# Performance work log

Measured on AMD Instinct MI355X. Metric: run time of the kernel, lower is better.

Reference implementation:

```python
import jax, jax.numpy as jnp
import numpy as np

N = 100_000          # nodes
E = 3_200_000        # edges (avg degree 32)
NEG_SLOPE = 0.2      # PyG GATConv default


def _gat_conv(x, src, dst, W, a_src, a_dst, b, n):
    """Single-head PyG-style GATConv. src/dst already include self-loops."""
    h = x @ W                                   # [N, F_out]
    logits = (h @ a_src)[src] + (h @ a_dst)[dst]  # [E']
    e = jax.nn.leaky_relu(logits, NEG_SLOPE)
    m = jax.ops.segment_max(e, dst, num_segments=n)
    ex = jnp.exp(e - m[dst])                    # stable ragged softmax over in-edges
    s = jax.ops.segment_sum(ex, dst, num_segments=n)
    alpha = ex / (s[dst] + 1e-16)
    out = jax.ops.segment_sum(h[src] * alpha[:, None], dst, num_segments=n)
    return out + b


def setup_inputs() -> dict:
    key = jax.random.key(0)
    ks = jax.random.split(key, 20)
    x = jax.random.normal(ks[0], (N, 3), dtype=jnp.float32)
    edge_index = jax.random.randint(ks[1], (2, E), 0, N, dtype=jnp.int64)

    def lin(k, fin, fout):
        return jax.random.normal(k, (fin, fout), dtype=jnp.float32) * (1.0 / np.sqrt(fin))

    def att(k, f):
        return jax.random.normal(k, (f,), dtype=jnp.float32) * (1.0 / np.sqrt(f))

    inp = {"x": x, "edge_index": edge_index}
    # forward-direction convs
    inp["W1"], inp["as1"], inp["ad1"], inp["b1"] = lin(ks[2], 3, 16), att(ks[3], 16), att(ks[4], 16), jnp.zeros((16,), jnp.float32)
    inp["W2"], inp["as2"], inp["ad2"], inp["b2"] = lin(ks[5], 16, 1), att(ks[6], 1), att(ks[7], 1), jnp.zeros((1,), jnp.float32)
    # reverse-direction convs
    inp["W1r"], inp["as1r"], inp["ad1r"], inp["b1r"] = lin(ks[8], 3, 16), att(ks[9], 16), att(ks[10], 16), jnp.zeros((16,), jnp.float32)
    inp["W2r"], inp["as2r"], inp["ad2r"], inp["b2r"] = lin(ks[11], 16, 1), att(ks[12], 1), att(ks[13], 1), jnp.zeros((1,), jnp.float32)
    return inp


def reference(x, edge_index, W1, as1, ad1, b1, W2, as2, ad2, b2,
              W1r, as1r, ad1r, b1r, W2r, as2r, ad2r, b2r):
    n = x.shape[0]
    loops = jnp.arange(n, dtype=edge_index.dtype)
    # forward direction (self-loops appended, as PyG add_self_loops=True)
    src = jnp.concatenate([edge_index[0], loops])
    dst = jnp.concatenate([edge_index[1], loops])
    # reverse direction: stack([ei[1], ei[0]]) then self-loops
    rsrc = jnp.concatenate([edge_index[1], loops])
    rdst = jnp.concatenate([edge_index[0], loops])

    xf = jax.nn.relu(_gat_conv(x, src, dst, W1, as1, ad1, b1, n))
    xf = _gat_conv(xf, src, dst, W2, as2, ad2, b2, n)

    xr = jax.nn.relu(_gat_conv(x, rsrc, rdst, W1r, as1r, ad1r, b1r, n))
    xr = _gat_conv(xr, rsrc, rdst, W2r, as2r, ad2r, b2r, n)

    return (xf + xr) * 0.5
```

## Files before the change

kernel.cpp:

```cpp
#include <hip/hip_runtime.h>
#include <math.h>

#define NSLOPE 0.2f
#define BSH 8
#define BNODES 256
#define NID_MASK 0x1FFFF
#define SENT 0xFFFFFFFFu
#define CAP 10240
#define GB 768
#define RE 2560
#define SLOT 12
#define SPILLCAP 256
#define BN9 512
#define LCAP 18432
#define BAGT 1024
#define CPP9 9

__device__ __forceinline__ float lrelu(float v) { return v > 0.f ? v : NSLOPE * v; }

__global__ void k_prep(const float* __restrict__ x,
                       const float* __restrict__ as1, const float* __restrict__ ad1,
                       const float* __restrict__ as1r, const float* __restrict__ ad1r,
                       const float* __restrict__ W1, const float* __restrict__ W1r,
                       float4* __restrict__ rec4f, float4* __restrict__ rec4r,
                       float* __restrict__ s1df, float* __restrict__ s1dr,
                       int* __restrict__ gcur, int NS, int N) {
    int i = blockIdx.x * blockDim.x + threadIdx.x;
    if (i < NS) gcur[i] = 0;
    if (i >= N) return;
    float x0 = x[3 * i], x1 = x[3 * i + 1], x2 = x[3 * i + 2];
    float ssf = 0.f, sdf = 0.f, ssr = 0.f, sdr = 0.f;
#pragma unroll
    for (int k = 0; k < 16; k++) {
        float hf = x0 * W1[k] + x1 * W1[16 + k] + x2 * W1[32 + k];
        ssf += hf * as1[k];
        sdf += hf * ad1[k];
        float hr = x0 * W1r[k] + x1 * W1r[16 + k] + x2 * W1r[32 + k];
        ssr += hr * as1r[k];
        sdr += hr * ad1r[k];
    }
    rec4f[i] = make_float4(x0, x1, x2, ssf);
    rec4r[i] = make_float4(x0, x1, x2, ssr);
    s1df[i] = sdf; s1dr[i] = sdr;
}

__global__ void __launch_bounds__(512) k_scatsort(
        const void* __restrict__ ei, long long E,
        int NB, int NS, int* __restrict__ gcur, unsigned* __restrict__ bin) {
    extern __shared__ unsigned smem[];
    unsigned* slots = smem;
    int* cnt  = (int*)(slots + (size_t)NS * SLOT);
    int* gpos = cnt + NS;
    int* spill_s = gpos + NS;
    int* spill_p = spill_s + SPILLCAP;
    unsigned* spill_r = (unsigned*)(spill_p + SPILLCAP);
    int* spn = (int*)(spill_r + SPILLCAP);
    __shared__ int flagsm;

    int t = threadIdx.x;
    if (t < 64) {
        const unsigned long long* p = (const unsigned long long*)ei;
        bool bad = false;
#pragma unroll
        for (int i = 0; i < 4; i++)
            if (p[t * 4 + i] >= (1ull << 32)) bad = true;
        unsigned long long mask = __ballot(bad);
        if (t == 0) flagsm = (mask == 0ull) ? 1 : 0;
    }
    __syncthreads();
    int fl = flagsm;
    long long chunk = (E + GB - 1) / GB;
    long long cstart = (long long)blockIdx.x * chunk;
    long long cend = cstart + chunk; if (cend > E) cend = E;

    for (long long rs = cstart; rs < cend; rs += RE) {
        int ne = (int)min((long long)RE, cend - rs);
        for (int c = t; c < NS; c += 512) cnt[c] = 0;
        if (t == 0) *spn = 0;
        __syncthreads();
#pragma unroll
        for (int k = 0; k < RE / 512; k++) {
            int idx = t + k * 512;
            if (idx < ne) {
                long long i = rs + idx;
                int u, v;
                if (fl) { const long long* p = (const long long*)ei; u = (int)p[i]; v = (int)p[E + i]; }
                else    { const int* p = (const int*)ei; u = p[i]; v = p[E + i]; }
                unsigned r0 = (unsigned)u | ((unsigned)(v & (BNODES - 1)) << 17);
                int s0 = v >> BSH;
                unsigned r1 = (unsigned)v | ((unsigned)(u & (BNODES - 1)) << 17);
                int s1 = NB + (u >> BSH);
                int p0 = atomicAdd(&cnt[s0], 1);
                if (p0 < SLOT) slots[s0 * SLOT + p0] = r0;
                else { int sp = atomicAdd(spn, 1); if (sp < SPILLCAP) { spill_s[sp] = s0; spill_p[sp] = p0; spill_r[sp] = r0; } }
                int p1 = atomicAdd(&cnt[s1], 1);
                if (p1 < SLOT) slots[s1 * SLOT + p1] = r1;
                else { int sp = atomicAdd(spn, 1); if (sp < SPILLCAP) { spill_s[sp] = s1; spill_p[sp] = p1; spill_r[sp] = r1; } }
            }
        }
        __syncthreads();
        for (int c = t; c < NS; c += 512) {
            int n = cnt[c];
            int rn = (n + 1) & ~1;
            gpos[c] = rn ? atomicAdd(&gcur[c], rn) : 0;
        }
        __syncthreads();
        for (int c = t; c < NS; c += 512) {
            int n = cnt[c];
            if (!n) continue;
            int rn = (n + 1) & ~1;
            int g = gpos[c];
            long long b = (long long)c * CAP;
            int m = n < SLOT ? n : SLOT;
            if (g + rn <= CAP) {
                uint2* bp = (uint2*)(bin + b + g);
                int np = (m + 1) >> 1;
                for (int j = 0; j < np; j++) {
                    unsigned v0 = slots[c * SLOT + 2 * j];
                    unsigned v1 = (2 * j + 1 < m) ? slots[c * SLOT + 2 * j + 1] : SENT;
                    bp[j] = make_uint2(v0, v1);
                }
                if (n > SLOT && rn > n)
                    bin[b + g + n] = SENT;
            }
        }
        int nsp = *spn; if (nsp > SPILLCAP) nsp = SPILLCAP;
        for (int i = t; i < nsp; i += 512) {
            int s = spill_s[i];
            int off = gpos[s] + spill_p[i];
            if (off < CAP) bin[(long long)s * CAP + off] = spill_r[i];
        }
        __syncthreads();
    }
}

__global__ void __launch_bounds__(BAGT, 8) k_bagg1(
        unsigned* __restrict__ bin, const int* __restrict__ gcur,
        const float4* __restrict__ rec4f, const float* __restrict__ s1df,
        const float4* __restrict__ rec4r, const float* __restrict__ s1dr,
        const float* __restrict__ b1, const float* __restrict__ W1,
        const float* __restrict__ W2,
        const float* __restrict__ as2, const float* __restrict__ ad2,
        const float* __restrict__ b1r, const float* __restrict__ W1r,
        const float* __restrict__ W2r,
        const float* __restrict__ as2r, const float* __restrict__ ad2r,
        float2* __restrict__ p2f, float* __restrict__ s2df,
        float2* __restrict__ p2r, float* __restrict__ s2dr,
        int* __restrict__ aoff, int* __restrict__ aend, int NB8, int N) {
    int bb = blockIdx.x, dir = blockIdx.y;
    const float4* rec4 = dir ? rec4r : rec4f;
    const float* s1d = dir ? s1dr : s1df;
    const float* b1_ = dir ? b1r : b1;
    const float* W1_ = dir ? W1r : W1;
    const float* W2_ = dir ? W2r : W2;
    float as2v = dir ? as2r[0] : as2[0];
    float ad2v = dir ? ad2r[0] : ad2[0];
    float2* p2 = dir ? p2r : p2f;
    float* s2d = dir ? s2dr : s2df;

    int c0 = dir * NB8 + 2 * bb;
    bool c1ok = (2 * bb + 1) < NB8;
    long long base = (long long)c0 * CAP;
    int n0 = gcur[c0]; if (n0 > CAP) n0 = CAP;
    int n1 = c1ok ? gcur[c0 + 1] : 0; if (n1 > CAP) n1 = CAP;
    int npair0 = n0 >> 1, npair1 = n1 >> 1;
    if (npair0 > LCAP / 2) npair0 = LCAP / 2;
    if (npair0 + npair1 > LCAP / 2) npair1 = LCAP / 2 - npair0;
    int nptot = npair0 + npair1;
    int v0 = bb << 9;
    int nv = N - v0; if (nv > BN9) nv = BN9;

    __shared__ int cnt[BN9];
    __shared__ int loff[BN9];
    __shared__ int segtot[8];
    __shared__ unsigned lds_u[LCAP];
    int t = threadIdx.x;

    const uint2* bp0 = (const uint2*)(bin + base);
    const uint2* bp1 = (const uint2*)(bin + base) + CAP / 2;
    uint2 recs[CPP9];
#pragma unroll
    for (int k = 0; k < CPP9; k++) {
        int i = t + k * BAGT;
        uint2 r = make_uint2(SENT, SENT);
        if (i < npair0) r = bp0[i];
        else if (i < nptot) {
            r = bp1[i - npair0];
            if (r.x != SENT) r.x += (256u << 17);
            if (r.y != SENT) r.y += (256u << 17);
        }
        recs[k] = r;
    }
    if (t < BN9) cnt[t] = 0;
    __syncthreads();
#pragma unroll
    for (int k = 0; k < CPP9; k++) {
        if (recs[k].x != SENT) atomicAdd(&cnt[recs[k].x >> 17], 1);
        if (recs[k].y != SENT) atomicAdd(&cnt[recs[k].y >> 17], 1);
    }
    __syncthreads();
    if (t < BN9) {
        int lane = t & 63, wv = t >> 6;
        int val = cnt[t];
        int incl = val;
#pragma unroll
        for (int od = 1; od < 64; od <<= 1) {
            int up = __shfl_up(incl, od);
            if (lane >= od) incl += up;
        }
        if (lane == 63) segtot[wv] = incl;
        loff[t] = incl - val;
    }
    __syncthreads();
    if (t < BN9) {
        int wv = t >> 6;
        int offs = 0;
#pragma unroll
        for (int j = 0; j < 8; j++) offs += (j < wv) ? segtot[j] : 0;
        int ex = loff[t] + offs;
        loff[t] = ex;
        cnt[t] = ex;
    }
    __syncthreads();
#pragma unroll
    for (int k = 0; k < CPP9; k++) {
        if (recs[k].x != SENT) {
            int p = atomicAdd(&cnt[recs[k].x >> 17], 1);
            lds_u[p] = recs[k].x & NID_MASK;
        }
        if (recs[k].y != SENT) {
            int p = atomicAdd(&cnt[recs[k].y >> 17], 1);
            lds_u[p] = recs[k].y & NID_MASK;
        }
    }
    __syncthreads();
    int node = t >> 1, lane = t & 1;
    float sdv = (node < nv) ? s1d[v0 + node] : 0.f;
    float d = 0.f, a0 = 0.f, a1 = 0.f, a2 = 0.f;
    if (node < nv) {
        int ls = loff[node], le = cnt[node];
        for (int pos = ls + lane; pos < le; pos += 2) {
            unsigned u = lds_u[pos];
            float4 r = rec4[u];
            float w = __expf(lrelu(r.w + sdv));
            d += w; a0 += w * r.x; a1 += w * r.y; a2 += w * r.z;
        }
    }
    d  += __shfl_xor(d, 1);
    a0 += __shfl_xor(a0, 1);
    a1 += __shfl_xor(a1, 1);
    a2 += __shfl_xor(a2, 1);
    if (lane == 0 && node < nv) {
        int v = v0 + node;
        float4 r = rec4[v];
        float w = __expf(lrelu(r.w + sdv));
        float dd = d + w;
        float inv = 1.f / (dd + 1e-16f);
        float m0 = (a0 + w * r.x) * inv;
        float m1 = (a1 + w * r.y) * inv;
        float m2 = (a2 + w * r.z) * inv;
        float h2v = 0.f;
#pragma unroll
        for (int k = 0; k < 16; k++) {
            float o = m0 * W1_[k] + m1 * W1_[16 + k] + m2 * W1_[32 + k] + b1_[k];
            o = fmaxf(o, 0.f);
            h2v += o * W2_[k];
        }
        p2[v] = make_float2(h2v, h2v * as2v);
        s2d[v] = h2v * ad2v;
    }
    int nreal = (nv > 0) ? cnt[nv - 1] : 0;
    if (t == 0 && (nreal & 1)) lds_u[nreal] = SENT;
    __syncthreads();
    int ndp = (nreal + 1) >> 1;
    uint2* bq = (uint2*)(bin + base);
    for (int i = t; i < ndp; i += BAGT)
        bq[i] = make_uint2(lds_u[2 * i], lds_u[2 * i + 1]);
    if (t < nv) {
        aoff[dir * N + v0 + t] = (int)(base + loff[t]);
        aend[dir * N + v0 + t] = (int)(base + cnt[t]);
    }
}

__global__ void k_agg2(const unsigned* __restrict__ bin,
                       const int* __restrict__ aoff, const int* __restrict__ aend,
                       const float2* __restrict__ p2f, const float* __restrict__ s2df,
                       const float2* __restrict__ p2r, const float* __restrict__ s2dr,
                       const float* __restrict__ b2, const float* __restrict__ b2r,
                       float* __restrict__ out, int N) {
    int tid = blockIdx.x * blockDim.x + threadIdx.x;
    int v = tid >> 3;
    int lane = tid & 7;
    if (v >= N) return;
    float res[2];
#pragma unroll
    for (int dir = 0; dir < 2; dir++) {
        const float2* p2 = dir ? p2r : p2f;
        const float* s2d = dir ? s2dr : s2df;
        float bias = dir ? b2r[0] : b2[0];
        float sd = s2d[v];
        int st = aoff[dir * N + v], en = aend[dir * N + v];
        float d = 0.f, a = 0.f;
        if (lane == 0) {
            float2 ts = p2[v];
            float w = __expf(lrelu(ts.y + sd));
            d = w; a = w * ts.x;
        }
        int j = st + lane;
        for (; j + 24 < en; j += 32) {
            unsigned u0 = __builtin_nontemporal_load(bin + j);
            unsigned u1 = __builtin_nontemporal_load(bin + j + 8);
            unsigned u2 = __builtin_nontemporal_load(bin + j + 16);
            unsigned u3 = __builtin_nontemporal_load(bin + j + 24);
            float2 t0 = p2[u0];
            float2 t1 = p2[u1];
            float2 t2 = p2[u2];
            float2 t3 = p2[u3];
            float w0 = __expf(lrelu(t0.y + sd));
            float w1 = __expf(lrelu(t1.y + sd));
            float w2 = __expf(lrelu(t2.y + sd));
            float w3 = __expf(lrelu(t3.y + sd));
            d += (w0 + w1) + (w2 + w3);
            a += w0 * t0.x + w1 * t1.x + w2 * t2.x + w3 * t3.x;
        }
        for (; j < en; j += 8) {
            unsigned u = __builtin_nontemporal_load(bin + j);
            float2 t = p2[u];
            float w = __expf(lrelu(t.y + sd));
            d += w;
            a += w * t.x;
        }
#pragma unroll
        for (int mask = 1; mask < 8; mask <<= 1) {
            d += __shfl_xor(d, mask);
            a += __shfl_xor(a, mask);
        }
        res[dir] = a / (d + 1e-16f) + bias;
    }
    if (lane == 0) out[v] = 0.5f * (res[0] + res[1]);
}

extern "C" void kernel_launch(void* const* d_in, const int* in_sizes, int n_in,
                              void* d_out, int out_size, void* d_ws, size_t ws_size,
                              hipStream_t stream) {
    const float* x   = (const float*)d_in[0];
    const void*  ei  = d_in[1];
    const float* W1  = (const float*)d_in[2];
    const float* as1 = (const float*)d_in[3];
    const float* ad1 = (const float*)d_in[4];
    const float* b1  = (const float*)d_in[5];
    const float* W2  = (const float*)d_in[6];
    const float* as2 = (const float*)d_in[7];
    const float* ad2 = (const float*)d_in[8];
    const float* b2  = (const float*)d_in[9];
    const float* W1r  = (const float*)d_in[10];
    const float* as1r = (const float*)d_in[11];
    const float* ad1r = (const float*)d_in[12];
    const float* b1r  = (const float*)d_in[13];
    const float* W2r  = (const float*)d_in[14];
    const float* as2r = (const float*)d_in[15];
    const float* ad2r = (const float*)d_in[16];
    const float* b2r  = (const float*)d_in[17];

    const int N = in_sizes[0] / 3;
    const long long E = in_sizes[1] / 2;
    const int NB8 = (N + BNODES - 1) >> BSH;
    const int NS = 2 * NB8;
    const int NB9 = (N + BN9 - 1) >> 9;

    char* w = (char*)d_ws;
    size_t o = 0;
    auto A = [&](size_t bytes) { o = (o + 255) & ~(size_t)255; size_t r = o; o += bytes; return r; };
    size_t oR4f  = A(sizeof(float4) * N);
    size_t oR4r  = A(sizeof(float4) * N);
    size_t oS1df = A(sizeof(float) * N);
    size_t oS1dr = A(sizeof(float) * N);
    size_t oP2f  = A(sizeof(float2) * N);
    size_t oS2df = A(sizeof(float) * N);
    size_t oP2r  = A(sizeof(float2) * N);
    size_t oS2dr = A(sizeof(float) * N);
    size_t oAoff = A(sizeof(int) * 2 * N);
    size_t oAend = A(sizeof(int) * 2 * N);
    size_t oGcur = A(sizeof(int) * NS);
    size_t oBin  = A(sizeof(unsigned) * (size_t)NS * CAP);
    (void)ws_size; (void)n_in; (void)out_size;

    float4* rec4f = (float4*)(w + oR4f);
    float4* rec4r = (float4*)(w + oR4r);
    float*  s1df = (float*)(w + oS1df);
    float*  s1dr = (float*)(w + oS1dr);
    float2* p2f  = (float2*)(w + oP2f);
    float*  s2df = (float*)(w + oS2df);
    float2* p2r  = (float2*)(w + oP2r);
    float*  s2dr = (float*)(w + oS2dr);
    int*    aoff = (int*)(w + oAoff);
    int*    aend = (int*)(w + oAend);
    int*    gcur = (int*)(w + oGcur);
    unsigned* bin = (unsigned*)(w + oBin);

    dim3 gN((N + 255) / 256);
    dim3 gAgg1(NB9, 2);
    dim3 gAgg2((N * 8 + 255) / 256);

    size_t smem = sizeof(unsigned) * (size_t)NS * SLOT
                + sizeof(int) * (size_t)NS * 2
                + sizeof(int) * SPILLCAP * 2
                + sizeof(unsigned) * SPILLCAP
                + 64;

    k_prep<<<gN, 256, 0, stream>>>(x, as1, ad1, as1r, ad1r, W1, W1r,
                                   rec4f, rec4r, s1df, s1dr, gcur, NS, N);
    k_scatsort<<<GB, 512, smem, stream>>>(ei, E, NB8, NS, gcur, bin);
    k_bagg1<<<gAgg1, BAGT, 0, stream>>>(bin, gcur, rec4f, s1df, rec4r, s1dr,
                                        b1, W1, W2, as2, ad2,
                                        b1r, W1r, W2r, as2r, ad2r,
                                        p2f, s2df, p2r, s2dr, aoff, aend, NB8, N);
    k_agg2<<<gAgg2, 256, 0, stream>>>(bin, aoff, aend, p2f, s2df, p2r, s2dr,
                                      b2, b2r, (float*)d_out, N);
}
```

Measured before the change: 234.9 us.

## Pack scatter bins densely and widen per-node aggregation to 16 lanes

The scatter-sort stops padding each block's per-bucket chunk to an even length, so no sentinel holes are written into the bins. Odd global offsets are handled with a scalar head and tail store. The segmented aggregator now masks the trailing odd element itself. Scatter grid, edges-per-block and slot sizes are retuned, and the final aggregation uses 16 lanes per node with 2-way unrolling instead of 8 lanes with 4-way. Denser bins mean fewer records to read and sort, at the cost of misaligned scalar stores and more lanes idle on low-degree nodes.

```diff
diff --git a/kernel.cpp b/kernel.cpp
--- a/kernel.cpp
+++ b/kernel.cpp
@@ -7,9 +7,9 @@
 #define NID_MASK 0x1FFFF
 #define SENT 0xFFFFFFFFu
 #define CAP 10240
-#define GB 768
-#define RE 2560
-#define SLOT 12
+#define GB 512
+#define RE 2048
+#define SLOT 10
 #define SPILLCAP 256
 #define BN9 512
 #define LCAP 18432
@@ -101,27 +101,22 @@
         __syncthreads();
         for (int c = t; c < NS; c += 512) {
             int n = cnt[c];
-            int rn = (n + 1) & ~1;
-            gpos[c] = rn ? atomicAdd(&gcur[c], rn) : 0;
+            gpos[c] = n ? atomicAdd(&gcur[c], n) : 0;
         }
         __syncthreads();
         for (int c = t; c < NS; c += 512) {
             int n = cnt[c];
             if (!n) continue;
-            int rn = (n + 1) & ~1;
             int g = gpos[c];
             long long b = (long long)c * CAP;
             int m = n < SLOT ? n : SLOT;
-            if (g + rn <= CAP) {
-                uint2* bp = (uint2*)(bin + b + g);
-                int np = (m + 1) >> 1;
-                for (int j = 0; j < np; j++) {
-                    unsigned v0 = slots[c * SLOT + 2 * j];
-                    unsigned v1 = (2 * j + 1 < m) ? slots[c * SLOT + 2 * j + 1] : SENT;
-                    bp[j] = make_uint2(v0, v1);
-                }
-                if (n > SLOT && rn > n)
-                    bin[b + g + n] = SENT;
+            if (g + n <= CAP) {
+                int j = 0;
+                if (g & 1) { bin[b + g] = slots[c * SLOT]; j = 1; }
+                for (; j + 2 <= m; j += 2)
+                    *(uint2*)(bin + b + g + j) =
+                        make_uint2(slots[c * SLOT + j], slots[c * SLOT + j + 1]);
+                if (j < m) bin[b + g + j] = slots[c * SLOT + j];
             }
         }
         int nsp = *spn; if (nsp > SPILLCAP) nsp = SPILLCAP;
@@ -163,10 +158,10 @@
     long long base = (long long)c0 * CAP;
     int n0 = gcur[c0]; if (n0 > CAP) n0 = CAP;
     int n1 = c1ok ? gcur[c0 + 1] : 0; if (n1 > CAP) n1 = CAP;
-    int npair0 = n0 >> 1, npair1 = n1 >> 1;
-    if (npair0 > LCAP / 2) npair0 = LCAP / 2;
-    if (npair0 + npair1 > LCAP / 2) npair1 = LCAP / 2 - npair0;
-    int nptot = npair0 + npair1;
+    int np0 = (n0 + 1) >> 1, np1 = (n1 + 1) >> 1;
+    if (np0 > LCAP / 2) np0 = LCAP / 2;
+    if (np0 + np1 > LCAP / 2) np1 = LCAP / 2 - np0;
+    int nptot = np0 + np1;
     int v0 = bb << 9;
     int nv = N - v0; if (nv > BN9) nv = BN9;
 
@@ -183,10 +178,14 @@
     for (int k = 0; k < CPP9; k++) {
         int i = t + k * BAGT;
         uint2 r = make_uint2(SENT, SENT);
-        if (i < npair0) r = bp0[i];
-        else if (i < nptot) {
-            r = bp1[i - npair0];
-            if (r.x != SENT) r.x += (256u << 17);
+        if (i < np0) {
+            r = bp0[i];
+            if (2 * i + 1 >= n0) r.y = SENT;
+        } else if (i < nptot) {
+            int i1 = i - np0;
+            r = bp1[i1];
+            if (2 * i1 + 1 >= n1) r.y = SENT;
+            r.x += (256u << 17);
             if (r.y != SENT) r.y += (256u << 17);
         }
         recs[k] = r;
@@ -289,8 +288,8 @@
                        const float* __restrict__ b2, const float* __restrict__ b2r,
                        float* __restrict__ out, int N) {
     int tid = blockIdx.x * blockDim.x + threadIdx.x;
-    int v = tid >> 3;
-    int lane = tid & 7;
+    int v = tid >> 4;
+    int lane = tid & 15;
     if (v >= N) return;
     float res[2];
 #pragma unroll
@@ -307,23 +306,17 @@
             d = w; a = w * ts.x;
         }
         int j = st + lane;
-        for (; j + 24 < en; j += 32) {
+        for (; j + 16 < en; j += 32) {
             unsigned u0 = __builtin_nontemporal_load(bin + j);
-            unsigned u1 = __builtin_nontemporal_load(bin + j + 8);
-            unsigned u2 = __builtin_nontemporal_load(bin + j + 16);
-            unsigned u3 = __builtin_nontemporal_load(bin + j + 24);
+            unsigned u1 = __builtin_nontemporal_load(bin + j + 16);
             float2 t0 = p2[u0];
             float2 t1 = p2[u1];
-            float2 t2 = p2[u2];
-            float2 t3 = p2[u3];
             float w0 = __expf(lrelu(t0.y + sd));
             float w1 = __expf(lrelu(t1.y + sd));
-            float w2 = __expf(lrelu(t2.y + sd));
-            float w3 = __expf(lrelu(t3.y + sd));
-            d += (w0 + w1) + (w2 + w3);
-            a += w0 * t0.x + w1 * t1.x + w2 * t2.x + w3 * t3.x;
-        }
-        for (; j < en; j += 8) {
+            d += w0 + w1;
+            a += w0 * t0.x + w1 * t1.x;
+        }
+        for (; j < en; j += 16) {
             unsigned u = __builtin_nontemporal_load(bin + j);
             float2 t = p2[u];
             float w = __expf(lrelu(t.y + sd));
@@ -331,7 +324,7 @@
             a += w * t.x;
         }
 #pragma unroll
-        for (int mask = 1; mask < 8; mask <<= 1) {
+        for (int mask = 1; mask < 16; mask <<= 1) {
             d += __shfl_xor(d, mask);
             a += __shfl_xor(a, mask);
         }
@@ -400,7 +393,7 @@
 
     dim3 gN((N + 255) / 256);
     dim3 gAgg1(NB9, 2);
-    dim3 gAgg2((N * 8 + 255) / 256);
+    dim3 gAgg2((N * 16 + 255) / 256);
 
     size_t smem = sizeof(unsigned) * (size_t)NS * SLOT
                 + sizeof(int) * (size_t)NS * 2
```

New measurement: 237.9 us. Within noise of the previous version (+1.3%).
